# Kernel tuning notes

Measured on AMD Instinct MI355X. Metric: run time of the kernel, lower is better.

The kernel has to match this reference:

```python
import jax, jax.numpy as jnp
import numpy as np

N, E, R, D, S = 50000, 400000, 500, 128, 20
P = R * S
EPS = 1e-5

def setup_inputs() -> dict:
    key = jax.random.key(0)
    ks = jax.random.split(key, 20)
    xav = (2.0 / (D + D)) ** 0.5  # xavier_normal std for square layers
    def W(k):
        return jax.random.normal(k, (D, D), jnp.float32) * xav
    inp = {
        'ent_emb': jax.random.normal(ks[0], (N, D), jnp.float32),
        'rel_emb': jax.random.normal(ks[1], (R, D), jnp.float32),
        'edge_Wo': W(ks[2]), 'edge_bo': jnp.zeros((D,), jnp.float32),
        'edge_Wi': W(ks[3]), 'edge_bi': jnp.zeros((D,), jnp.float32),
        'edge_g': jnp.ones((D,), jnp.float32), 'edge_b': jnp.zeros((D,), jnp.float32),
        'node_Wo': W(ks[4]), 'node_bo': jnp.zeros((D,), jnp.float32),
        'node_Wi': W(ks[5]), 'node_bi': jnp.zeros((D,), jnp.float32),
        'node_g': jnp.ones((D,), jnp.float32), 'node_b': jnp.zeros((D,), jnp.float32),
        'comp_Wo': W(ks[6]), 'comp_bo': jnp.zeros((D,), jnp.float32),
        'comp_Wi': W(ks[7]), 'comp_bi': jnp.zeros((D,), jnp.float32),
        'comp_g': jnp.ones((D,), jnp.float32), 'comp_b': jnp.zeros((D,), jnp.float32),
        'relW': W(ks[8]), 'relb': jnp.zeros((D,), jnp.float32),
        'src': jax.random.randint(ks[9], (E,), 0, N),
        'dst': jax.random.randint(ks[10], (E,), 0, N),
        'etype': jax.random.randint(ks[11], (E,), 0, R),
        'heads': jax.random.randint(ks[13], (P,), 0, N),
        'tails': jax.random.randint(ks[14], (P,), 0, N),
        'rel_ids': jnp.repeat(jnp.arange(R), S),  # S sampled pairs per relation
    }
    in_mask = jax.random.randint(ks[12], (E,), 0, 2).astype(bool)
    inp['in_mask'] = in_mask
    inp['out_mask'] = ~in_mask  # DGL forward/reverse edge split: complementary masks
    return inp

def _edge_softmax(logit, dst, n):
    # segment softmax over edges grouped by destination node
    m = jax.ops.segment_max(logit, dst, num_segments=n)
    e = jnp.exp(logit - m[dst])
    s = jax.ops.segment_sum(e, dst, num_segments=n)
    return e / s[dst]

def _in_out(x, in_m, out_m, Wo, bo, Wi, bi):
    ho = x @ Wo.T + bo
    hi = x @ Wi.T + bi
    h = jnp.where(out_m[:, None], ho, jnp.zeros((), x.dtype))
    return jnp.where(in_m[:, None], hi, h)  # in-edges overwrite (masks disjoint)

def _bn_tanh(x, g, b):
    # training-mode BatchNorm1d (biased batch variance) + Tanh
    mu = jnp.mean(x, 0)
    var = jnp.mean(jnp.square(x - mu), 0)
    return jnp.tanh(g * (x - mu) * jax.lax.rsqrt(var + EPS) + b)

def reference(ent_emb, rel_emb,
              edge_Wo, edge_bo, edge_Wi, edge_bi, edge_g, edge_b,
              node_Wo, node_bo, node_Wi, node_bi, node_g, node_b,
              comp_Wo, comp_bo, comp_Wi, comp_bi, comp_g, comp_b,
              relW, relb,
              src, dst, etype, in_mask, out_mask, heads, tails, rel_ids):
    n = ent_emb.shape[0]
    r = rel_emb.shape[0]
    rel_e = rel_emb[etype]      # [E,D]
    e_src = ent_emb[src]        # [E,D]
    e_dst = ent_emb[dst]        # [E,D]

    # EdgeLayer: attn = e_dot_v(rel_e, dst_emb)
    a = _edge_softmax(jnp.sum(rel_e * e_dst, -1), dst, n)
    h = _in_out(rel_e, in_mask, out_mask, edge_Wo, edge_bo, edge_Wi, edge_bi) * a[:, None]
    edge_ent = _bn_tanh(jax.ops.segment_sum(h, dst, num_segments=n), edge_g, edge_b)

    # NodeLayer: attn = u_dot_v, message = src emb
    a = _edge_softmax(jnp.sum(e_src * e_dst, -1), dst, n)
    h = _in_out(e_src, in_mask, out_mask, node_Wo, node_bo, node_Wi, node_bi) * a[:, None]
    node_ent = _bn_tanh(jax.ops.segment_sum(h, dst, num_segments=n), node_g, node_b)

    # CompLayer (comp_fn='mul'): comp = u_mul_e, attn = e_dot_v(comp, dst)
    comp = e_src * rel_e
    a = _edge_softmax(jnp.sum(comp * e_dst, -1), dst, n)
    h = _in_out(comp, in_mask, out_mask, comp_Wo, comp_bo, comp_Wi, comp_bi) * a[:, None]
    comp_ent = _bn_tanh(jax.ops.segment_sum(h, dst, num_segments=n), comp_g, comp_b)

    final_ent = comp_ent + ent_emb + edge_ent + node_ent

    # update_relations: mean of w_rel_edge(tail - head) per relation
    pair = ent_emb[tails] - ent_emb[heads]          # [P,D]
    upd = pair @ relW.T + relb
    ssum = jax.ops.segment_sum(upd, rel_ids, num_segments=r)
    cnt = jax.ops.segment_sum(jnp.ones((rel_ids.shape[0],), jnp.float32), rel_ids, num_segments=r)
    cnt = jnp.maximum(cnt, 1.0)[:, None]
    final_rel = rel_emb + jnp.tanh(ssum / cnt)
    return final_ent, final_rel
```

## Files before the change

### kernel.cpp

```cpp
#include <hip/hip_runtime.h>
#include <stdint.h>

#define DN 128

typedef short s16x8 __attribute__((ext_vector_type(8)));
typedef float f32x4 __attribute__((ext_vector_type(4)));

__device__ __forceinline__ float bfs(unsigned short u){ return __uint_as_float(((uint32_t)u) << 16); }
__device__ __forceinline__ uint32_t f2bf(float f){
    uint32_t x = __float_as_uint(f);
    return (x + 0x7FFFu + ((x >> 16) & 1u)) >> 16;
}
__device__ __forceinline__ uint32_t packbf(float a, float b){ return f2bf(a) | (f2bf(b) << 16); }
__device__ __forceinline__ float tanh_(float x){
    float e = __expf(2.0f * x);
    return 1.0f - 2.0f / (e + 1.0f);
}

__global__ void k_detect(const uint32_t* mask, int nwords, int* flag){
    __shared__ int sh;
    if (threadIdx.x == 0) sh = 0;
    __syncthreads();
    int bad = 0;
    for (int i = threadIdx.x; i < nwords; i += blockDim.x)
        if (mask[i] > 1u) bad = 1;
    if (bad) atomicOr(&sh, 1);
    __syncthreads();
    if (threadIdx.x == 0) *flag = sh;
}

struct WC { const float* src[6]; };
__global__ void k_wcvt(WC wc, unsigned short* dstp){
    int i = blockIdx.x * 256 + threadIdx.x;
    int m = i >> 14, o = i & 16383;
    dstp[(size_t)m * 16384 + o] = (unsigned short)f2bf(wc.src[m][o]);
}

__global__ void k_hist(const int* dst, int* counts, int E){
    int e = blockIdx.x * blockDim.x + threadIdx.x;
    if (e < E) atomicAdd(&counts[dst[e]], 1);
}
__global__ void k_scan_a(const int* counts, int* bsums){
    int t = threadIdx.x;
    int s = counts[blockIdx.x * 256 + t];
    #pragma unroll
    for (int o = 32; o; o >>= 1) s += __shfl_xor(s, o);
    __shared__ int wsum[4];
    if ((t & 63) == 0) wsum[t >> 6] = s;
    __syncthreads();
    if (t == 0) bsums[blockIdx.x] = wsum[0] + wsum[1] + wsum[2] + wsum[3];
}
__global__ void k_scan_b(int* bsums, int nb){
    __shared__ int buf[256];
    int t = threadIdx.x;
    int v = (t < nb) ? bsums[t] : 0;
    buf[t] = v; __syncthreads();
    for (int o = 1; o < 256; o <<= 1){
        int add = (t >= o) ? buf[t - o] : 0;
        __syncthreads();
        buf[t] += add;
        __syncthreads();
    }
    if (t < nb) bsums[t] = buf[t] - v;
}
__global__ void k_scan_c(const int* counts, const int* bsums, int* rowst, int* cursor, int npad, int E){
    __shared__ int buf[256];
    int t = threadIdx.x, i = blockIdx.x * 256 + t;
    int c = counts[i];
    buf[t] = c; __syncthreads();
    for (int o = 1; o < 256; o <<= 1){
        int add = (t >= o) ? buf[t - o] : 0;
        __syncthreads();
        buf[t] += add;
        __syncthreads();
    }
    int rsv = buf[t] - c + bsums[blockIdx.x];
    rowst[i] = rsv; cursor[i] = rsv;
    if (i == npad - 1) rowst[npad] = E;
}
__global__ void k_scatter(const int* dst, int* cursor, int* eord, int E){
    int e = blockIdx.x * blockDim.x + threadIdx.x;
    if (e < E){ int pos = atomicAdd(&cursor[dst[e]], 1); eord[pos] = e; }
}

__global__ __launch_bounds__(256)
void k_node(const float2* ent2, const float2* rel2,
            const int* src, const int* etype,
            const unsigned char* mask8, const int* flagp,
            const int* rowst, const int* eord,
            uint32_t* Sw, float* Rv, int Nn, int npad)
{
    int t = threadIdx.x, lane = t & 63, wv = t >> 6;
    int v = blockIdx.x * 4 + wv;
    if (v >= npad) return;
    int bmode = *flagp;
    const int* mask32 = (const int*)mask8;

    float dx = 0.f, dy = 0.f; int deg = 0, rs = 0;
    if (v < Nn){
        rs = rowst[v]; deg = rowst[v + 1] - rs;
        float2 dw = ent2[(size_t)v * 64 + lane];
        dx = dw.x; dy = dw.y;
    }
    float m0=-1e30f, m1=-1e30f, m2=-1e30f;
    float si0=0,si1=0,si2=0, so0=0,so1=0,so2=0;
    float ai0x=0,ai0y=0,ao0x=0,ao0y=0;
    float ai1x=0,ai1y=0,ao1x=0,ao1y=0;
    float ai2x=0,ai2y=0,ao2x=0,ao2y=0;

    for (int base = 0; base < deg; base += 64){
        int nb = min(64, deg - base);
        int sv = 0, tv = 0, mk = 0;
        if (lane < nb){
            int eid = eord[rs + base + lane];
            sv = src[eid]; tv = etype[eid];
            mk = bmode ? (int)mask8[eid] : mask32[eid];
        }
        for (int j = 0; j < nb; ++j){
            int sj = __shfl(sv, j), tj = __shfl(tv, j), mj = __shfl(mk, j);
            float2 sw = ent2[(size_t)sj * 64 + lane];
            float2 rw = rel2[(size_t)tj * 64 + lane];
            float sx = sw.x, sy = sw.y, rx = rw.x, ry = rw.y;
            float cx = sx * rx, cy = sy * ry;
            float p0 = rx * dx + ry * dy;
            float p1 = sx * dx + sy * dy;
            float p2 = cx * dx + cy * dy;
            #pragma unroll
            for (int o = 32; o; o >>= 1){
                p0 += __shfl_xor(p0, o);
                p1 += __shfl_xor(p1, o);
                p2 += __shfl_xor(p2, o);
            }
            { float nm = fmaxf(m0, p0), f = __expf(m0 - nm), e = __expf(p0 - nm);
              si0*=f; so0*=f; ai0x*=f; ai0y*=f; ao0x*=f; ao0y*=f;
              if (mj){ si0+=e; ai0x+=e*rx; ai0y+=e*ry; } else { so0+=e; ao0x+=e*rx; ao0y+=e*ry; }
              m0 = nm; }
            { float nm = fmaxf(m1, p1), f = __expf(m1 - nm), e = __expf(p1 - nm);
              si1*=f; so1*=f; ai1x*=f; ai1y*=f; ao1x*=f; ao1y*=f;
              if (mj){ si1+=e; ai1x+=e*sx; ai1y+=e*sy; } else { so1+=e; ao1x+=e*sx; ao1y+=e*sy; }
              m1 = nm; }
            { float nm = fmaxf(m2, p2), f = __expf(m2 - nm), e = __expf(p2 - nm);
              si2*=f; so2*=f; ai2x*=f; ai2y*=f; ao2x*=f; ao2y*=f;
              if (mj){ si2+=e; ai2x+=e*cx; ai2y+=e*cy; } else { so2+=e; ao2x+=e*cx; ao2y+=e*cy; }
              m2 = nm; }
        }
    }
    size_t sstr = (size_t)npad * 64;
    size_t widx = (size_t)v * 64 + lane;
    float st, inv;
    st = si0 + so0; inv = st > 0.f ? 1.f / st : 0.f;
    Sw[0*sstr + widx] = packbf(ai0x*inv, ai0y*inv);
    Sw[1*sstr + widx] = packbf(ao0x*inv, ao0y*inv);
    float ri0 = si0*inv, ro0 = so0*inv;
    st = si1 + so1; inv = st > 0.f ? 1.f / st : 0.f;
    Sw[2*sstr + widx] = packbf(ai1x*inv, ai1y*inv);
    Sw[3*sstr + widx] = packbf(ao1x*inv, ao1y*inv);
    float ri1 = si1*inv, ro1 = so1*inv;
    st = si2 + so2; inv = st > 0.f ? 1.f / st : 0.f;
    Sw[4*sstr + widx] = packbf(ai2x*inv, ai2y*inv);
    Sw[5*sstr + widx] = packbf(ao2x*inv, ao2y*inv);
    float ri2 = si2*inv, ro2 = so2*inv;
    if (lane == 0){
        Rv[0*(size_t)npad + v] = ri0; Rv[1*(size_t)npad + v] = ro0;
        Rv[2*(size_t)npad + v] = ri1; Rv[3*(size_t)npad + v] = ro1;
        Rv[4*(size_t)npad + v] = ri2; Rv[5*(size_t)npad + v] = ro2;
    }
}

struct GArgs {
    const short* Wi[3]; const short* Wo[3];
    const float* bi[3]; const float* bo[3];
};

__global__ __launch_bounds__(256)
void k_gemm(GArgs ga, const short* Sb, const float* Rv, unsigned short* P, float* stats,
            int npad, int Nn)
{
    __shared__ float lsum[128], lsq[128];
    int t = threadIdx.x;
    if (t < 128){ lsum[t] = 0.f; lsq[t] = 0.f; }
    __syncthreads();
    int l = blockIdx.y;
    int lane = t & 63, wv = t >> 6;
    int lo = lane & 15, hi = lane >> 4;
    int r0 = blockIdx.x * 64 + wv * 16;
    size_t sstride = (size_t)npad * DN;
    const short* Sin  = Sb + (size_t)(2*l)   * sstride;
    const short* Sout = Sb + (size_t)(2*l+1) * sstride;
    const short* Wi = ga.Wi[l]; const short* Wo = ga.Wo[l];

    s16x8 ain[4], aout[4];
    #pragma unroll
    for (int kb = 0; kb < 4; ++kb){
        size_t o = (size_t)(r0 + lo) * DN + kb*32 + hi*8;
        ain[kb]  = *(const s16x8*)(Sin + o);
        aout[kb] = *(const s16x8*)(Sout + o);
    }
    float rin[4], rout[4];
    const float* RvI = Rv + (size_t)(2*l)   * npad;
    const float* RvO = Rv + (size_t)(2*l+1) * npad;
    #pragma unroll
    for (int rg = 0; rg < 4; ++rg){
        int vr = r0 + hi*4 + rg;
        rin[rg] = RvI[vr]; rout[rg] = RvO[vr];
    }
    unsigned short* Pl = P + (size_t)l * sstride;

    #pragma unroll
    for (int ct = 0; ct < 8; ++ct){
        f32x4 acc = {0.f, 0.f, 0.f, 0.f};
        #pragma unroll
        for (int kb = 0; kb < 4; ++kb){
            size_t wo = (size_t)(ct*16 + lo) * DN + kb*32 + hi*8;
            s16x8 bwi = *(const s16x8*)(Wi + wo);
            acc = __builtin_amdgcn_mfma_f32_16x16x32_bf16(ain[kb], bwi, acc, 0, 0, 0);
            s16x8 bwo = *(const s16x8*)(Wo + wo);
            acc = __builtin_amdgcn_mfma_f32_16x16x32_bf16(aout[kb], bwo, acc, 0, 0, 0);
        }
        int j = ct*16 + lo;
        float biv = ga.bi[l][j], bov = ga.bo[l][j];
        float cs = 0.f, cq = 0.f;
        #pragma unroll
        for (int rg = 0; rg < 4; ++rg){
            float pv = acc[rg] + rin[rg]*biv + rout[rg]*bov;
            Pl[(size_t)(r0 + hi*4 + rg) * DN + j] = (unsigned short)f2bf(pv);
            cs += pv; cq += pv*pv;
        }
        cs += __shfl_xor(cs, 16); cs += __shfl_xor(cs, 32);
        cq += __shfl_xor(cq, 16); cq += __shfl_xor(cq, 32);
        if (lane < 16){ atomicAdd(&lsum[j], cs); atomicAdd(&lsq[j], cq); }
    }
    __syncthreads();
    if (t < 128){
        atomicAdd(&stats[l*128 + t], lsum[t]);
        atomicAdd(&stats[384 + l*128 + t], lsq[t]);
    }
}

struct BArgs { const float* g[3]; const float* b[3]; };

__global__ void k_bn(BArgs ba, const float* stats, float* bnAB, int Nn){
    int t = threadIdx.x;
    if (t >= 384) return;
    int l = t >> 7, j = t & 127;
    float su = stats[t], sq = stats[384 + t];
    float mu = su / (float)Nn;
    float var = fmaxf(sq / (float)Nn - mu*mu, 0.f);
    float inv = rsqrtf(var + 1e-5f);
    float g = ba.g[l][j], b = ba.b[l][j];
    bnAB[t] = g * inv;
    bnAB[384 + t] = b - mu * g * inv;
}

__global__ void k_final(const unsigned short* Pb, const float* bnAB, const float* ent,
                        float* outp, int Nn, int npad)
{
    int gid = blockIdx.x * blockDim.x + threadIdx.x;
    if (gid >= Nn * 32) return;
    int v = gid >> 5, q4 = (gid & 31) * 4;
    size_t pst = (size_t)npad * DN;
    size_t pb = (size_t)v * DN + q4;
    ushort4 p0 = *(const ushort4*)(Pb + pb);
    ushort4 p1 = *(const ushort4*)(Pb + pst + pb);
    ushort4 p2 = *(const ushort4*)(Pb + 2*pst + pb);
    float4 e4 = *(const float4*)(ent + (size_t)v * DN + q4);
    float pe[4] = { e4.x, e4.y, e4.z, e4.w };
    unsigned short pu[3][4] = { {p0.x, p0.y, p0.z, p0.w},
                                {p1.x, p1.y, p1.z, p1.w},
                                {p2.x, p2.y, p2.z, p2.w} };
    float o[4];
    #pragma unroll
    for (int q = 0; q < 4; ++q){
        float s = pe[q];
        #pragma unroll
        for (int l = 0; l < 3; ++l){
            int jj = l*128 + q4 + q;
            s += tanh_(bnAB[jj] * bfs(pu[l][q]) + bnAB[384 + jj]);
        }
        o[q] = s;
    }
    float4 ov = { o[0], o[1], o[2], o[3] };
    *(float4*)(outp + (size_t)v * DN + q4) = ov;
}

__global__ void k_rel(const float* ent, const float* relW, const float* relb,
                      const float* rel, const int* heads, const int* tails,
                      float* outr, int Sp)
{
    __shared__ float mp[128];
    int r = blockIdx.x, j = threadIdx.x;
    float acc = 0.f;
    for (int s = 0; s < Sp; ++s){
        int p = r * Sp + s;
        int hh = heads[p], tt = tails[p];
        acc += ent[(size_t)tt * DN + j] - ent[(size_t)hh * DN + j];
    }
    mp[j] = acc / (float)Sp;
    __syncthreads();
    float dot = relb[j];
    const float4* wr = (const float4*)(relW + (size_t)j * DN);
    #pragma unroll 8
    for (int kb = 0; kb < 32; ++kb){
        float4 w = wr[kb];
        dot += mp[kb*4+0]*w.x + mp[kb*4+1]*w.y + mp[kb*4+2]*w.z + mp[kb*4+3]*w.w;
    }
    outr[(size_t)r * DN + j] = rel[(size_t)r * DN + j] + tanh_(dot);
}

extern "C" void kernel_launch(void* const* d_in, const int* in_sizes, int n_in,
                              void* d_out, int out_size, void* d_ws, size_t ws_size,
                              hipStream_t stream)
{
    const float* entf = (const float*)d_in[0];
    const float* relf = (const float*)d_in[1];
    const float* eWo = (const float*)d_in[2];  const float* ebo = (const float*)d_in[3];
    const float* eWi = (const float*)d_in[4];  const float* ebi = (const float*)d_in[5];
    const float* eg  = (const float*)d_in[6];  const float* eb  = (const float*)d_in[7];
    const float* nWo = (const float*)d_in[8];  const float* nbo = (const float*)d_in[9];
    const float* nWi = (const float*)d_in[10]; const float* nbi = (const float*)d_in[11];
    const float* ng  = (const float*)d_in[12]; const float* nb_ = (const float*)d_in[13];
    const float* cWo = (const float*)d_in[14]; const float* cbo = (const float*)d_in[15];
    const float* cWi = (const float*)d_in[16]; const float* cbi = (const float*)d_in[17];
    const float* cg  = (const float*)d_in[18]; const float* cb  = (const float*)d_in[19];
    const float* relWs  = (const float*)d_in[20];
    const float* relb32 = (const float*)d_in[21];
    const int* srcp   = (const int*)d_in[22];
    const int* dstp   = (const int*)d_in[23];
    const int* etyp   = (const int*)d_in[24];
    const int* headsp = (const int*)d_in[25];
    const int* tailsp = (const int*)d_in[26];
    const unsigned char* mask8 = (const unsigned char*)d_in[28];

    int Nn = in_sizes[0] / DN;
    int Rr = in_sizes[1] / DN;
    int E  = in_sizes[22];
    int Pp = in_sizes[25];
    int Sp = Pp / Rr;
    int npad = ((Nn + 255) / 256) * 256;
    int nsb = npad / 256;

    char* w = (char*)d_ws; size_t off = 0;
    auto carve = [&](size_t b) -> void* {
        void* p = w + off; off = (off + b + 255) & ~(size_t)255; return p;
    };
    int*   flag   = (int*)  carve(4);
    int*   counts = (int*)  carve((size_t)npad * 4);
    int*   rowst  = (int*)  carve((size_t)(npad + 1) * 4);
    int*   cursor = (int*)  carve((size_t)npad * 4);
    int*   eord   = (int*)  carve((size_t)E * 4);
    int*   bsums  = (int*)  carve(1024 * 4);
    unsigned short* wcv = (unsigned short*)carve((size_t)6 * 16384 * 2);
    short* Sb     = (short*)carve((size_t)6 * npad * DN * 2);
    unsigned short* Pb = (unsigned short*)carve((size_t)3 * npad * DN * 2);
    float* Rv     = (float*)carve((size_t)6 * npad * 4);
    float* stats  = (float*)carve(1024 * 4);
    float* bnAB   = (float*)carve(1024 * 4);

    hipMemsetAsync(counts, 0, (size_t)npad * 4, stream);
    hipMemsetAsync(stats, 0, 1024 * 4, stream);

    int nw = E / 4; if (nw > 4096) nw = 4096;
    k_detect<<<1, 256, 0, stream>>>((const uint32_t*)mask8, nw, flag);

    WC wc; wc.src[0] = eWi; wc.src[1] = nWi; wc.src[2] = cWi;
           wc.src[3] = eWo; wc.src[4] = nWo; wc.src[5] = cWo;
    k_wcvt<<<384, 256, 0, stream>>>(wc, wcv);

    k_hist<<<(E + 255) / 256, 256, 0, stream>>>(dstp, counts, E);
    k_scan_a<<<nsb, 256, 0, stream>>>(counts, bsums);
    k_scan_b<<<1, 256, 0, stream>>>(bsums, nsb);
    k_scan_c<<<nsb, 256, 0, stream>>>(counts, bsums, rowst, cursor, npad, E);
    k_scatter<<<(E + 255) / 256, 256, 0, stream>>>(dstp, cursor, eord, E);

    k_node<<<npad / 4, 256, 0, stream>>>((const float2*)entf, (const float2*)relf,
                                         srcp, etyp, mask8, flag,
                                         rowst, eord, (uint32_t*)Sb, Rv, Nn, npad);

    GArgs ga;
    ga.Wi[0] = (const short*)(wcv + 0*16384);
    ga.Wi[1] = (const short*)(wcv + 1*16384);
    ga.Wi[2] = (const short*)(wcv + 2*16384);
    ga.Wo[0] = (const short*)(wcv + 3*16384);
    ga.Wo[1] = (const short*)(wcv + 4*16384);
    ga.Wo[2] = (const short*)(wcv + 5*16384);
    ga.bi[0] = ebi; ga.bi[1] = nbi; ga.bi[2] = cbi;
    ga.bo[0] = ebo; ga.bo[1] = nbo; ga.bo[2] = cbo;
    k_gemm<<<dim3(npad / 64, 3), 256, 0, stream>>>(ga, Sb, Rv, Pb, stats, npad, Nn);

    BArgs ba;
    ba.g[0] = eg; ba.g[1] = ng; ba.g[2] = cg;
    ba.b[0] = eb; ba.b[1] = nb_; ba.b[2] = cb;
    k_bn<<<1, 384, 0, stream>>>(ba, stats, bnAB, Nn);

    float* outF = (float*)d_out;
    k_final<<<(Nn * 32 + 255) / 256, 256, 0, stream>>>(Pb, bnAB, entf, outF, Nn, npad);

    k_rel<<<Rr, 128, 0, stream>>>(entf, relWs, relb32, relf, headsp, tailsp,
                                  outF + (size_t)Nn * DN, Sp);
}
```

Measured before the change: 419.8 us.

## Fuse setup kernels, pack edge metadata, and process two edges per wave in node kernel

Merges mask detection, weight conversion and histogram into one pre-kernel, folds the two scan stages into one, and merges BN finalization, final output and relation update into a single launch. The scatter now packs src, etype and mask into one 32-bit word per edge, so the node kernel reads one coalesced word instead of three dependent gathers. The node kernel splits each wave into two half-waves that each handle one edge with float4 loads, then merges the two online-softmax states at the end. This cuts launch count and gather latency. The packing assumes src fits in 16 bits and etype in 15 bits, and pairs Rr/2 relations per block, which assumes Rr is even.

```diff
diff --git a/kernel.cpp b/kernel.cpp
--- a/kernel.cpp
+++ b/kernel.cpp
@@ -17,29 +17,19 @@
     return 1.0f - 2.0f / (e + 1.0f);
 }
 
-__global__ void k_detect(const uint32_t* mask, int nwords, int* flag){
-    __shared__ int sh;
-    if (threadIdx.x == 0) sh = 0;
-    __syncthreads();
-    int bad = 0;
-    for (int i = threadIdx.x; i < nwords; i += blockDim.x)
-        if (mask[i] > 1u) bad = 1;
-    if (bad) atomicOr(&sh, 1);
-    __syncthreads();
-    if (threadIdx.x == 0) *flag = sh;
-}
-
 struct WC { const float* src[6]; };
-__global__ void k_wcvt(WC wc, unsigned short* dstp){
-    int i = blockIdx.x * 256 + threadIdx.x;
-    int m = i >> 14, o = i & 16383;
-    dstp[(size_t)m * 16384 + o] = (unsigned short)f2bf(wc.src[m][o]);
-}
-
-__global__ void k_hist(const int* dst, int* counts, int E){
-    int e = blockIdx.x * blockDim.x + threadIdx.x;
-    if (e < E) atomicAdd(&counts[dst[e]], 1);
-}
+__global__ void k_pre(const int* dst, int* counts,
+                      const uint32_t* maskw, int nwords, int* flag,
+                      WC wc, unsigned short* wcv, int E){
+    int gid = blockIdx.x * 256 + threadIdx.x;
+    if (gid < E) atomicAdd(&counts[dst[gid]], 1);
+    if (gid < nwords && maskw[gid] > 1u) atomicOr(flag, 1);
+    if (gid < 6 * 16384){
+        int m = gid >> 14, o = gid & 16383;
+        wcv[(size_t)m * 16384 + o] = (unsigned short)f2bf(wc.src[m][o]);
+    }
+}
+
 __global__ void k_scan_a(const int* counts, int* bsums){
     int t = threadIdx.x;
     int s = counts[blockIdx.x * 256 + t];
@@ -50,120 +40,177 @@
     __syncthreads();
     if (t == 0) bsums[blockIdx.x] = wsum[0] + wsum[1] + wsum[2] + wsum[3];
 }
-__global__ void k_scan_b(int* bsums, int nb){
+
+__global__ void k_scan_bc(const int* counts, const int* bsums, int nsb,
+                          int* rowst, int* cursor, int npad, int E){
+    __shared__ int pref;
+    __shared__ int wsum[4];
     __shared__ int buf[256];
-    int t = threadIdx.x;
-    int v = (t < nb) ? bsums[t] : 0;
-    buf[t] = v; __syncthreads();
+    int t = threadIdx.x, bid = blockIdx.x;
+    int s = (t < bid && t < nsb) ? bsums[t] : 0;
+    #pragma unroll
+    for (int o = 32; o; o >>= 1) s += __shfl_xor(s, o);
+    if ((t & 63) == 0) wsum[t >> 6] = s;
+    __syncthreads();
+    if (t == 0) pref = wsum[0] + wsum[1] + wsum[2] + wsum[3];
+    int i = bid * 256 + t;
+    int c = counts[i];
+    buf[t] = c;
+    __syncthreads();
     for (int o = 1; o < 256; o <<= 1){
         int add = (t >= o) ? buf[t - o] : 0;
         __syncthreads();
         buf[t] += add;
         __syncthreads();
     }
-    if (t < nb) bsums[t] = buf[t] - v;
-}
-__global__ void k_scan_c(const int* counts, const int* bsums, int* rowst, int* cursor, int npad, int E){
-    __shared__ int buf[256];
-    int t = threadIdx.x, i = blockIdx.x * 256 + t;
-    int c = counts[i];
-    buf[t] = c; __syncthreads();
-    for (int o = 1; o < 256; o <<= 1){
-        int add = (t >= o) ? buf[t - o] : 0;
-        __syncthreads();
-        buf[t] += add;
-        __syncthreads();
-    }
-    int rsv = buf[t] - c + bsums[blockIdx.x];
+    int rsv = buf[t] - c + pref;
     rowst[i] = rsv; cursor[i] = rsv;
     if (i == npad - 1) rowst[npad] = E;
 }
-__global__ void k_scatter(const int* dst, int* cursor, int* eord, int E){
+
+__global__ void k_scatter(const int* dst, const int* src, const int* etype,
+                          const unsigned char* mask8, const int* flagp,
+                          int* cursor, uint32_t* epack, int E){
     int e = blockIdx.x * blockDim.x + threadIdx.x;
-    if (e < E){ int pos = atomicAdd(&cursor[dst[e]], 1); eord[pos] = e; }
+    if (e >= E) return;
+    int bmode = *flagp;
+    int mk = bmode ? (int)mask8[e] : ((const int*)mask8)[e];
+    int pos = atomicAdd(&cursor[dst[e]], 1);
+    epack[pos] = ((uint32_t)src[e] << 16) | ((uint32_t)etype[e] << 1) | (uint32_t)(mk != 0);
 }
 
 __global__ __launch_bounds__(256)
-void k_node(const float2* ent2, const float2* rel2,
-            const int* src, const int* etype,
-            const unsigned char* mask8, const int* flagp,
-            const int* rowst, const int* eord,
+void k_node(const float4* ent4, const float4* rel4,
+            const uint32_t* epack, const int* rowst,
             uint32_t* Sw, float* Rv, int Nn, int npad)
 {
     int t = threadIdx.x, lane = t & 63, wv = t >> 6;
     int v = blockIdx.x * 4 + wv;
     if (v >= npad) return;
-    int bmode = *flagp;
-    const int* mask32 = (const int*)mask8;
-
-    float dx = 0.f, dy = 0.f; int deg = 0, rs = 0;
+    int sl = lane & 31, half = lane >> 5;
+
+    float4 d4 = {0.f, 0.f, 0.f, 0.f};
+    int deg = 0, rs = 0;
     if (v < Nn){
         rs = rowst[v]; deg = rowst[v + 1] - rs;
-        float2 dw = ent2[(size_t)v * 64 + lane];
-        dx = dw.x; dy = dw.y;
-    }
-    float m0=-1e30f, m1=-1e30f, m2=-1e30f;
-    float si0=0,si1=0,si2=0, so0=0,so1=0,so2=0;
-    float ai0x=0,ai0y=0,ao0x=0,ao0y=0;
-    float ai1x=0,ai1y=0,ao1x=0,ao1y=0;
-    float ai2x=0,ai2y=0,ao2x=0,ao2y=0;
+        d4 = ent4[(size_t)v * 32 + sl];
+    }
+    float m0 = -1e30f, m1 = -1e30f, m2 = -1e30f;
+    float si0 = 0, si1 = 0, si2 = 0, so0 = 0, so1 = 0, so2 = 0;
+    float4 aI0 = {0,0,0,0}, aO0 = {0,0,0,0};
+    float4 aI1 = {0,0,0,0}, aO1 = {0,0,0,0};
+    float4 aI2 = {0,0,0,0}, aO2 = {0,0,0,0};
 
     for (int base = 0; base < deg; base += 64){
         int nb = min(64, deg - base);
-        int sv = 0, tv = 0, mk = 0;
-        if (lane < nb){
-            int eid = eord[rs + base + lane];
-            sv = src[eid]; tv = etype[eid];
-            mk = bmode ? (int)mask8[eid] : mask32[eid];
-        }
-        for (int j = 0; j < nb; ++j){
-            int sj = __shfl(sv, j), tj = __shfl(tv, j), mj = __shfl(mk, j);
-            float2 sw = ent2[(size_t)sj * 64 + lane];
-            float2 rw = rel2[(size_t)tj * 64 + lane];
-            float sx = sw.x, sy = sw.y, rx = rw.x, ry = rw.y;
-            float cx = sx * rx, cy = sy * ry;
-            float p0 = rx * dx + ry * dy;
-            float p1 = sx * dx + sy * dy;
-            float p2 = cx * dx + cy * dy;
+        uint32_t pk = 0;
+        if (lane < nb) pk = epack[rs + base + lane];
+        int npair = (nb + 1) >> 1;
+        for (int j = 0; j < npair; ++j){
+            int ei = 2 * j + half;
+            uint32_t w = (uint32_t)__shfl((int)pk, ei);
+            int sj = (int)(w >> 16);
+            int tj = (int)((w >> 1) & 0x7FFF);
+            float mk = (float)(w & 1u);
+            bool pad = (ei >= nb);
+            float4 s4 = ent4[(size_t)sj * 32 + sl];
+            float4 r4 = rel4[(size_t)tj * 32 + sl];
+            float4 c4 = { s4.x*r4.x, s4.y*r4.y, s4.z*r4.z, s4.w*r4.w };
+            float p0 = r4.x*d4.x + r4.y*d4.y + r4.z*d4.z + r4.w*d4.w;
+            float p1 = s4.x*d4.x + s4.y*d4.y + s4.z*d4.z + s4.w*d4.w;
+            float p2 = c4.x*d4.x + c4.y*d4.y + c4.z*d4.z + c4.w*d4.w;
             #pragma unroll
-            for (int o = 32; o; o >>= 1){
+            for (int o = 1; o < 32; o <<= 1){
                 p0 += __shfl_xor(p0, o);
                 p1 += __shfl_xor(p1, o);
                 p2 += __shfl_xor(p2, o);
             }
-            { float nm = fmaxf(m0, p0), f = __expf(m0 - nm), e = __expf(p0 - nm);
-              si0*=f; so0*=f; ai0x*=f; ai0y*=f; ao0x*=f; ao0y*=f;
-              if (mj){ si0+=e; ai0x+=e*rx; ai0y+=e*ry; } else { so0+=e; ao0x+=e*rx; ao0y+=e*ry; }
-              m0 = nm; }
-            { float nm = fmaxf(m1, p1), f = __expf(m1 - nm), e = __expf(p1 - nm);
-              si1*=f; so1*=f; ai1x*=f; ai1y*=f; ao1x*=f; ao1y*=f;
-              if (mj){ si1+=e; ai1x+=e*sx; ai1y+=e*sy; } else { so1+=e; ao1x+=e*sx; ao1y+=e*sy; }
-              m1 = nm; }
-            { float nm = fmaxf(m2, p2), f = __expf(m2 - nm), e = __expf(p2 - nm);
-              si2*=f; so2*=f; ai2x*=f; ai2y*=f; ao2x*=f; ao2y*=f;
-              if (mj){ si2+=e; ai2x+=e*cx; ai2y+=e*cy; } else { so2+=e; ao2x+=e*cx; ao2y+=e*cy; }
-              m2 = nm; }
-        }
-    }
-    size_t sstr = (size_t)npad * 64;
-    size_t widx = (size_t)v * 64 + lane;
-    float st, inv;
-    st = si0 + so0; inv = st > 0.f ? 1.f / st : 0.f;
-    Sw[0*sstr + widx] = packbf(ai0x*inv, ai0y*inv);
-    Sw[1*sstr + widx] = packbf(ao0x*inv, ao0y*inv);
-    float ri0 = si0*inv, ro0 = so0*inv;
-    st = si1 + so1; inv = st > 0.f ? 1.f / st : 0.f;
-    Sw[2*sstr + widx] = packbf(ai1x*inv, ai1y*inv);
-    Sw[3*sstr + widx] = packbf(ao1x*inv, ao1y*inv);
-    float ri1 = si1*inv, ro1 = so1*inv;
-    st = si2 + so2; inv = st > 0.f ? 1.f / st : 0.f;
-    Sw[4*sstr + widx] = packbf(ai2x*inv, ai2y*inv);
-    Sw[5*sstr + widx] = packbf(ao2x*inv, ao2y*inv);
-    float ri2 = si2*inv, ro2 = so2*inv;
-    if (lane == 0){
-        Rv[0*(size_t)npad + v] = ri0; Rv[1*(size_t)npad + v] = ro0;
-        Rv[2*(size_t)npad + v] = ri1; Rv[3*(size_t)npad + v] = ro1;
-        Rv[4*(size_t)npad + v] = ri2; Rv[5*(size_t)npad + v] = ro2;
+            if (pad){ p0 = -1e38f; p1 = -1e38f; p2 = -1e38f; }
+            {
+                float nm = fmaxf(m0, p0);
+                float f = __expf(m0 - nm);
+                si0 *= f; so0 *= f;
+                aI0.x*=f; aI0.y*=f; aI0.z*=f; aI0.w*=f;
+                aO0.x*=f; aO0.y*=f; aO0.z*=f; aO0.w*=f;
+                m0 = nm;
+                float e = __expf(p0 - m0);
+                float ein = e * mk, eout = e - ein;
+                si0 += ein; so0 += eout;
+                aI0.x += ein*r4.x; aI0.y += ein*r4.y; aI0.z += ein*r4.z; aI0.w += ein*r4.w;
+                aO0.x += eout*r4.x; aO0.y += eout*r4.y; aO0.z += eout*r4.z; aO0.w += eout*r4.w;
+            }
+            {
+                float nm = fmaxf(m1, p1);
+                float f = __expf(m1 - nm);
+                si1 *= f; so1 *= f;
+                aI1.x*=f; aI1.y*=f; aI1.z*=f; aI1.w*=f;
+                aO1.x*=f; aO1.y*=f; aO1.z*=f; aO1.w*=f;
+                m1 = nm;
+                float e = __expf(p1 - m1);
+                float ein = e * mk, eout = e - ein;
+                si1 += ein; so1 += eout;
+                aI1.x += ein*s4.x; aI1.y += ein*s4.y; aI1.z += ein*s4.z; aI1.w += ein*s4.w;
+                aO1.x += eout*s4.x; aO1.y += eout*s4.y; aO1.z += eout*s4.z; aO1.w += eout*s4.w;
+            }
+            {
+                float nm = fmaxf(m2, p2);
+                float f = __expf(m2 - nm);
+                si2 *= f; so2 *= f;
+                aI2.x*=f; aI2.y*=f; aI2.z*=f; aI2.w*=f;
+                aO2.x*=f; aO2.y*=f; aO2.z*=f; aO2.w*=f;
+                m2 = nm;
+                float e = __expf(p2 - m2);
+                float ein = e * mk, eout = e - ein;
+                si2 += ein; so2 += eout;
+                aI2.x += ein*c4.x; aI2.y += ein*c4.y; aI2.z += ein*c4.z; aI2.w += ein*c4.w;
+                aO2.x += eout*c4.x; aO2.y += eout*c4.y; aO2.z += eout*c4.z; aO2.w += eout*c4.w;
+            }
+        }
+    }
+
+    {
+        float mo, nm, f;
+#define MRG(m, si, so, aI, aO)                                            \
+        mo = __shfl_xor(m, 32);                                           \
+        nm = fmaxf(m, mo);                                                \
+        f = __expf(m - nm);                                               \
+        si *= f; so *= f;                                                 \
+        aI.x*=f; aI.y*=f; aI.z*=f; aI.w*=f;                               \
+        aO.x*=f; aO.y*=f; aO.z*=f; aO.w*=f;                               \
+        si += __shfl_xor(si, 32);                                         \
+        so += __shfl_xor(so, 32);                                         \
+        aI.x += __shfl_xor(aI.x, 32); aI.y += __shfl_xor(aI.y, 32);       \
+        aI.z += __shfl_xor(aI.z, 32); aI.w += __shfl_xor(aI.w, 32);       \
+        aO.x += __shfl_xor(aO.x, 32); aO.y += __shfl_xor(aO.y, 32);       \
+        aO.z += __shfl_xor(aO.z, 32); aO.w += __shfl_xor(aO.w, 32);
+        MRG(m0, si0, so0, aI0, aO0)
+        MRG(m1, si1, so1, aI1, aO1)
+        MRG(m2, si2, so2, aI2, aO2)
+#undef MRG
+    }
+
+    if (half == 0){
+        uint2* S2 = (uint2*)Sw;
+        size_t s2 = (size_t)npad * 32;
+        size_t wi = (size_t)v * 32 + sl;
+        float st, inv;
+        st = si0 + so0; inv = st > 0.f ? 1.f / st : 0.f;
+        S2[0*s2 + wi] = make_uint2(packbf(aI0.x*inv, aI0.y*inv), packbf(aI0.z*inv, aI0.w*inv));
+        S2[1*s2 + wi] = make_uint2(packbf(aO0.x*inv, aO0.y*inv), packbf(aO0.z*inv, aO0.w*inv));
+        float ri0 = si0*inv, ro0 = so0*inv;
+        st = si1 + so1; inv = st > 0.f ? 1.f / st : 0.f;
+        S2[2*s2 + wi] = make_uint2(packbf(aI1.x*inv, aI1.y*inv), packbf(aI1.z*inv, aI1.w*inv));
+        S2[3*s2 + wi] = make_uint2(packbf(aO1.x*inv, aO1.y*inv), packbf(aO1.z*inv, aO1.w*inv));
+        float ri1 = si1*inv, ro1 = so1*inv;
+        st = si2 + so2; inv = st > 0.f ? 1.f / st : 0.f;
+        S2[4*s2 + wi] = make_uint2(packbf(aI2.x*inv, aI2.y*inv), packbf(aI2.z*inv, aI2.w*inv));
+        S2[5*s2 + wi] = make_uint2(packbf(aO2.x*inv, aO2.y*inv), packbf(aO2.z*inv, aO2.w*inv));
+        float ri2 = si2*inv, ro2 = so2*inv;
+        if (sl == 0){
+            Rv[0*(size_t)npad + v] = ri0; Rv[1*(size_t)npad + v] = ro0;
+            Rv[2*(size_t)npad + v] = ri1; Rv[3*(size_t)npad + v] = ro1;
+            Rv[4*(size_t)npad + v] = ri2; Rv[5*(size_t)npad + v] = ro2;
+        }
     }
 }
 
@@ -237,74 +284,75 @@
     }
 }
 
-struct BArgs { const float* g[3]; const float* b[3]; };
-
-__global__ void k_bn(BArgs ba, const float* stats, float* bnAB, int Nn){
-    int t = threadIdx.x;
-    if (t >= 384) return;
-    int l = t >> 7, j = t & 127;
-    float su = stats[t], sq = stats[384 + t];
-    float mu = su / (float)Nn;
-    float var = fmaxf(sq / (float)Nn - mu*mu, 0.f);
-    float inv = rsqrtf(var + 1e-5f);
-    float g = ba.g[l][j], b = ba.b[l][j];
-    bnAB[t] = g * inv;
-    bnAB[384 + t] = b - mu * g * inv;
-}
-
-__global__ void k_final(const unsigned short* Pb, const float* bnAB, const float* ent,
-                        float* outp, int Nn, int npad)
+struct FArgs { const float* g[3]; const float* b[3]; };
+
+__global__ __launch_bounds__(256)
+void k_fin(const unsigned short* Pb, const float* stats, FArgs fa,
+           const float* ent, const float* relW, const float* relb,
+           const float* rel, const int* heads, const int* tails,
+           float* outp, int Nn, int npad, int FB, int Sp)
 {
-    int gid = blockIdx.x * blockDim.x + threadIdx.x;
-    if (gid >= Nn * 32) return;
-    int v = gid >> 5, q4 = (gid & 31) * 4;
-    size_t pst = (size_t)npad * DN;
-    size_t pb = (size_t)v * DN + q4;
-    ushort4 p0 = *(const ushort4*)(Pb + pb);
-    ushort4 p1 = *(const ushort4*)(Pb + pst + pb);
-    ushort4 p2 = *(const ushort4*)(Pb + 2*pst + pb);
-    float4 e4 = *(const float4*)(ent + (size_t)v * DN + q4);
-    float pe[4] = { e4.x, e4.y, e4.z, e4.w };
-    unsigned short pu[3][4] = { {p0.x, p0.y, p0.z, p0.w},
-                                {p1.x, p1.y, p1.z, p1.w},
-                                {p2.x, p2.y, p2.z, p2.w} };
-    float o[4];
-    #pragma unroll
-    for (int q = 0; q < 4; ++q){
-        float s = pe[q];
+    int t = threadIdx.x, bid = blockIdx.x;
+    if (bid < FB){
+        __shared__ float sAB[768];
+        for (int i = t; i < 384; i += 256){
+            int l = i >> 7;
+            float su = stats[i], sq = stats[384 + i];
+            float mu = su / (float)Nn;
+            float var = fmaxf(sq / (float)Nn - mu*mu, 0.f);
+            float inv = rsqrtf(var + 1e-5f);
+            float g = fa.g[l][i & 127], b = fa.b[l][i & 127];
+            sAB[i] = g * inv;
+            sAB[384 + i] = b - mu * g * inv;
+        }
+        __syncthreads();
+        int gid = bid * 256 + t;
+        if (gid >= Nn * 32) return;
+        int v = gid >> 5, q4 = (gid & 31) * 4;
+        size_t pst = (size_t)npad * DN;
+        size_t pb = (size_t)v * DN + q4;
+        ushort4 p0 = *(const ushort4*)(Pb + pb);
+        ushort4 p1 = *(const ushort4*)(Pb + pst + pb);
+        ushort4 p2 = *(const ushort4*)(Pb + 2*pst + pb);
+        float4 e4 = *(const float4*)(ent + (size_t)v * DN + q4);
+        float pe[4] = { e4.x, e4.y, e4.z, e4.w };
+        unsigned short pu[3][4] = { {p0.x, p0.y, p0.z, p0.w},
+                                    {p1.x, p1.y, p1.z, p1.w},
+                                    {p2.x, p2.y, p2.z, p2.w} };
+        float o[4];
         #pragma unroll
-        for (int l = 0; l < 3; ++l){
-            int jj = l*128 + q4 + q;
-            s += tanh_(bnAB[jj] * bfs(pu[l][q]) + bnAB[384 + jj]);
-        }
-        o[q] = s;
-    }
-    float4 ov = { o[0], o[1], o[2], o[3] };
-    *(float4*)(outp + (size_t)v * DN + q4) = ov;
-}
-
-__global__ void k_rel(const float* ent, const float* relW, const float* relb,
-                      const float* rel, const int* heads, const int* tails,
-                      float* outr, int Sp)
-{
-    __shared__ float mp[128];
-    int r = blockIdx.x, j = threadIdx.x;
-    float acc = 0.f;
-    for (int s = 0; s < Sp; ++s){
-        int p = r * Sp + s;
-        int hh = heads[p], tt = tails[p];
-        acc += ent[(size_t)tt * DN + j] - ent[(size_t)hh * DN + j];
-    }
-    mp[j] = acc / (float)Sp;
-    __syncthreads();
-    float dot = relb[j];
-    const float4* wr = (const float4*)(relW + (size_t)j * DN);
-    #pragma unroll 8
-    for (int kb = 0; kb < 32; ++kb){
-        float4 w = wr[kb];
-        dot += mp[kb*4+0]*w.x + mp[kb*4+1]*w.y + mp[kb*4+2]*w.z + mp[kb*4+3]*w.w;
-    }
-    outr[(size_t)r * DN + j] = rel[(size_t)r * DN + j] + tanh_(dot);
+        for (int q = 0; q < 4; ++q){
+            float s = pe[q];
+            #pragma unroll
+            for (int l = 0; l < 3; ++l){
+                int jj = l*128 + q4 + q;
+                s += tanh_(sAB[jj] * bfs(pu[l][q]) + sAB[384 + jj]);
+            }
+            o[q] = s;
+        }
+        float4 ov = { o[0], o[1], o[2], o[3] };
+        *(float4*)(outp + (size_t)v * DN + q4) = ov;
+    } else {
+        __shared__ float mp[256];
+        int rr = (bid - FB) * 2 + (t >> 7);
+        int j = t & 127;
+        float acc = 0.f;
+        for (int s = 0; s < Sp; ++s){
+            int p = rr * Sp + s;
+            acc += ent[(size_t)tails[p] * DN + j] - ent[(size_t)heads[p] * DN + j];
+        }
+        mp[t] = acc / (float)Sp;
+        __syncthreads();
+        float dot = relb[j];
+        const float4* wr = (const float4*)(relW + (size_t)j * DN);
+        const float* mpr = mp + (t >> 7) * 128;
+        #pragma unroll 8
+        for (int kb = 0; kb < 32; ++kb){
+            float4 w = wr[kb];
+            dot += mpr[kb*4+0]*w.x + mpr[kb*4+1]*w.y + mpr[kb*4+2]*w.z + mpr[kb*4+3]*w.w;
+        }
+        outp[(size_t)Nn * DN + (size_t)rr * DN + j] = rel[(size_t)rr * DN + j] + tanh_(dot);
+    }
 }
 
 extern "C" void kernel_launch(void* const* d_in, const int* in_sizes, int n_in,
@@ -345,36 +393,31 @@
     };
     int*   flag   = (int*)  carve(4);
     int*   counts = (int*)  carve((size_t)npad * 4);
+    float* stats  = (float*)carve(1024 * 4);
+    size_t zlen = off;
     int*   rowst  = (int*)  carve((size_t)(npad + 1) * 4);
     int*   cursor = (int*)  carve((size_t)npad * 4);
-    int*   eord   = (int*)  carve((size_t)E * 4);
+    uint32_t* epack = (uint32_t*)carve((size_t)E * 4);
     int*   bsums  = (int*)  carve(1024 * 4);
     unsigned short* wcv = (unsigned short*)carve((size_t)6 * 16384 * 2);
     short* Sb     = (short*)carve((size_t)6 * npad * DN * 2);
     unsigned short* Pb = (unsigned short*)carve((size_t)3 * npad * DN * 2);
     float* Rv     = (float*)carve((size_t)6 * npad * 4);
-    float* stats  = (float*)carve(1024 * 4);
-    float* bnAB   = (float*)carve(1024 * 4);
-
-    hipMemsetAsync(counts, 0, (size_t)npad * 4, stream);
-    hipMemsetAsync(stats, 0, 1024 * 4, stream);
-
-    int nw = E / 4; if (nw > 4096) nw = 4096;
-    k_detect<<<1, 256, 0, stream>>>((const uint32_t*)mask8, nw, flag);
+
+    hipMemsetAsync(d_ws, 0, zlen, stream);
 
     WC wc; wc.src[0] = eWi; wc.src[1] = nWi; wc.src[2] = cWi;
            wc.src[3] = eWo; wc.src[4] = nWo; wc.src[5] = cWo;
-    k_wcvt<<<384, 256, 0, stream>>>(wc, wcv);
-
-    k_hist<<<(E + 255) / 256, 256, 0, stream>>>(dstp, counts, E);
+    int nwords = 4096;
+    k_pre<<<(E + 255) / 256, 256, 0, stream>>>(dstp, counts, (const uint32_t*)mask8,
+                                               nwords, flag, wc, wcv, E);
     k_scan_a<<<nsb, 256, 0, stream>>>(counts, bsums);
-    k_scan_b<<<1, 256, 0, stream>>>(bsums, nsb);
-    k_scan_c<<<nsb, 256, 0, stream>>>(counts, bsums, rowst, cursor, npad, E);
-    k_scatter<<<(E + 255) / 256, 256, 0, stream>>>(dstp, cursor, eord, E);
-
-    k_node<<<npad / 4, 256, 0, stream>>>((const float2*)entf, (const float2*)relf,
-                                         srcp, etyp, mask8, flag,
-                                         rowst, eord, (uint32_t*)Sb, Rv, Nn, npad);
+    k_scan_bc<<<nsb, 256, 0, stream>>>(counts, bsums, nsb, rowst, cursor, npad, E);
+    k_scatter<<<(E + 255) / 256, 256, 0, stream>>>(dstp, srcp, etyp, mask8, flag,
+                                                   cursor, epack, E);
+
+    k_node<<<npad / 4, 256, 0, stream>>>((const float4*)entf, (const float4*)relf,
+                                         epack, rowst, (uint32_t*)Sb, Rv, Nn, npad);
 
     GArgs ga;
     ga.Wi[0] = (const short*)(wcv + 0*16384);
@@ -387,14 +430,11 @@
     ga.bo[0] = ebo; ga.bo[1] = nbo; ga.bo[2] = cbo;
     k_gemm<<<dim3(npad / 64, 3), 256, 0, stream>>>(ga, Sb, Rv, Pb, stats, npad, Nn);
 
-    BArgs ba;
-    ba.g[0] = eg; ba.g[1] = ng; ba.g[2] = cg;
-    ba.b[0] = eb; ba.b[1] = nb_; ba.b[2] = cb;
-    k_bn<<<1, 384, 0, stream>>>(ba, stats, bnAB, Nn);
-
-    float* outF = (float*)d_out;
-    k_final<<<(Nn * 32 + 255) / 256, 256, 0, stream>>>(Pb, bnAB, entf, outF, Nn, npad);
-
-    k_rel<<<Rr, 128, 0, stream>>>(entf, relWs, relb32, relf, headsp, tailsp,
-                                  outF + (size_t)Nn * DN, Sp);
-}
+    FArgs fa;
+    fa.g[0] = eg; fa.g[1] = ng; fa.g[2] = cg;
+    fa.b[0] = eb; fa.b[1] = nb_; fa.b[2] = cb;
+    int FB = (Nn * 32 + 255) / 256;
+    int grid = FB + Rr / 2;
+    k_fin<<<grid, 256, 0, stream>>>(Pb, stats, fa, entf, relWs, relb32, relf,
+                                    headsp, tailsp, (float*)d_out, Nn, npad, FB, Sp);
+}
```

Measured after the change: 393.7 us. -6.2%, faster.
